# Optimization experiments

Hardware: AMD Instinct MI355X
Metric: run time of the kernel (lower is better)

Reference implementation:

```python
import jax, jax.numpy as jnp
import numpy as np

H = 1024

def _gru_layer(x_seq, W_ih, W_hh, b_ih, b_hh):
    # x_seq: [B, T, in]; W_ih: [3H, in]; W_hh: [3H, H]
    B = x_seq.shape[0]
    gx = jnp.einsum('bti,gi->btg', x_seq, W_ih) + b_ih  # [B, T, 3H] input gates precomputed

    def step(h, gx_t):
        gh = h @ W_hh.T + b_hh  # [B, 3H]
        xr, xz, xn = jnp.split(gx_t, 3, axis=-1)
        hr, hz, hn = jnp.split(gh, 3, axis=-1)
        r = jax.nn.sigmoid(xr + hr)
        z = jax.nn.sigmoid(xz + hz)
        n = jnp.tanh(xn + r * hn)
        h_new = (1.0 - z) * n + z * h
        return h_new, h_new

    h0 = jnp.zeros((B, W_hh.shape[1]), dtype=x_seq.dtype)
    _, out = jax.lax.scan(step, h0, jnp.swapaxes(gx, 0, 1))  # scan over T
    return jnp.swapaxes(out, 0, 1)  # [B, T, H]

def setup_inputs() -> dict:
    key = jax.random.key(0)
    ks = jax.random.split(key, 8)
    s = 0.03  # ~1/sqrt(H) init scale to avoid gate saturation
    return {
        'tokens': jax.random.randint(ks[0], (16, 1024), 0, 32000),
        'emb': jax.random.normal(ks[1], (32000, H), jnp.float32),
        'W_ih_l0': jax.random.normal(ks[2], (3 * H, H), jnp.float32) * s,
        'W_hh_l0': jax.random.normal(ks[3], (3 * H, H), jnp.float32) * s,
        'b_ih_l0': jnp.zeros((3 * H,), jnp.float32),
        'b_hh_l0': jnp.zeros((3 * H,), jnp.float32),
        'W_ih_l1': jax.random.normal(ks[4], (3 * H, H), jnp.float32) * s,
        'W_hh_l1': jax.random.normal(ks[5], (3 * H, H), jnp.float32) * s,
        'b_ih_l1': jnp.zeros((3 * H,), jnp.float32),
        'b_hh_l1': jnp.zeros((3 * H,), jnp.float32),
        'W_lin': jax.random.normal(ks[6], (128, H), jnp.float32) * s,
        'b_lin': jnp.zeros((128,), jnp.float32),
    }

def reference(tokens, emb, W_ih_l0, W_hh_l0, b_ih_l0, b_hh_l0,
              W_ih_l1, W_hh_l1, b_ih_l1, b_hh_l1, W_lin, b_lin):
    x = emb[tokens]  # [B, T, H]
    h1 = _gru_layer(x, W_ih_l0, W_hh_l0, b_ih_l0, b_hh_l0)
    h2 = _gru_layer(h1, W_ih_l1, W_hh_l1, b_ih_l1, b_hh_l1)
    logits = jnp.einsum('bth,ch->btc', h2, W_lin) + b_lin  # [B, T, C]
    # F.log_softmax with no dim on a 3D tensor uses dim=1 (PyTorch deprecated default)
    return jax.nn.log_softmax(logits, axis=1)
```

## Files before the change

### kernel.cpp

```cpp
#include <hip/hip_runtime.h>
#include <stdint.h>

typedef unsigned short u16;
typedef unsigned int u32;
typedef unsigned long long u64;
typedef __attribute__((ext_vector_type(8))) short short8;
typedef __attribute__((ext_vector_type(4))) float f32x4;

#define T_SEQ 1024
#define HDIM  1024
#define NG    3072
#define SLOT  16384
#define FSTRIDE 32

__device__ __forceinline__ u16 f2bf(float f) {
  unsigned u = __float_as_uint(f);
  u += 0x7FFF + ((u >> 16) & 1);
  return (u16)(u >> 16);
}
__device__ __forceinline__ float bf2f(u16 h) {
  return __uint_as_float(((unsigned)h) << 16);
}

__device__ __forceinline__ int prow(int b) { return b ^ ((b >> 2) & 1); }

__device__ __forceinline__ void gld16(void* lds, const void* g) {
  __builtin_amdgcn_global_load_lds(
      (const __attribute__((address_space(1))) unsigned*)g,
      (__attribute__((address_space(3))) unsigned*)lds, 16, 0, 0);
}

__device__ __forceinline__ void st_agent_u32(unsigned* p, unsigned v) {
  __hip_atomic_store(p, v, __ATOMIC_RELAXED, __HIP_MEMORY_SCOPE_AGENT);
}
__device__ __forceinline__ void st_agent_u64(u64* p, u64 v) {
  __hip_atomic_store(p, v, __ATOMIC_RELAXED, __HIP_MEMORY_SCOPE_AGENT);
}
__device__ __forceinline__ unsigned ld_agent_u32(const unsigned* p) {
  return __hip_atomic_load(p, __ATOMIC_RELAXED, __HIP_MEMORY_SCOPE_AGENT);
}

__device__ __forceinline__ void poll64(const unsigned* flags, int wave, int lane, unsigned need) {
  const unsigned* f = flags + (size_t)(16 * wave + (lane >> 2)) * FSTRIDE + (lane & 3);
  while (ld_agent_u32(f) < need) {}
  asm volatile("" ::: "memory");
}

__global__ void cast5_kernel(const float* __restrict__ s0, const float* __restrict__ s1,
                             const float* __restrict__ s2, const float* __restrict__ s3,
                             const float* __restrict__ s4,
                             u16* __restrict__ d0, u16* __restrict__ d1,
                             u16* __restrict__ d2, u16* __restrict__ d3,
                             u16* __restrict__ d4, unsigned* __restrict__ flags) {
  if (blockIdx.x == 0) {
#pragma unroll
    for (int k = 0; k < 64; ++k) flags[threadIdx.x * 64 + k] = 0;
  }
  int bid = blockIdx.x;
  const float* s; u16* d; size_t base;
  if (bid < 3072)       { s = s0; d = d0; base = (size_t)bid * 1024; }
  else if (bid < 6144)  { s = s1; d = d1; base = (size_t)(bid - 3072) * 1024; }
  else if (bid < 9216)  { s = s2; d = d2; base = (size_t)(bid - 6144) * 1024; }
  else if (bid < 12288) { s = s3; d = d3; base = (size_t)(bid - 9216) * 1024; }
  else                  { s = s4; d = d4; base = (size_t)(bid - 12288) * 1024; }
  size_t i = base + (size_t)threadIdx.x * 4;
  float4 v = *(const float4*)(s + i);
  unsigned lo = (unsigned)f2bf(v.x) | ((unsigned)f2bf(v.y) << 16);
  unsigned hi = (unsigned)f2bf(v.z) | ((unsigned)f2bf(v.w) << 16);
  uint2 o; o.x = lo; o.y = hi;
  *(uint2*)(d + i) = o;
}

__global__ void gather_cast_kernel(const int* __restrict__ tokens,
                                   const float* __restrict__ emb,
                                   u16* __restrict__ xbf) {
  int row = blockIdx.x;
  int tok = tokens[row];
  const float4* src = (const float4*)(emb + (size_t)tok * HDIM);
  float4 v = src[threadIdx.x];
  unsigned lo = (unsigned)f2bf(v.x) | ((unsigned)f2bf(v.y) << 16);
  unsigned hi = (unsigned)f2bf(v.z) | ((unsigned)f2bf(v.w) << 16);
  uint2 o; o.x = lo; o.y = hi;
  *(uint2*)(xbf + (size_t)row * HDIM + (size_t)threadIdx.x * 4) = o;
}

template <int OUT_MODE, bool A_PACKED, bool ADD_BIAS>
__global__ __launch_bounds__(256)
void gemm_bt(const u16* __restrict__ A, const u16* __restrict__ Bt,
             void* __restrict__ Cout, const float* __restrict__ bias,
             int M, int N) {
  const int K = 1024;
  __shared__ u16 As[128 * 32];
  __shared__ u16 Bs[128 * 32];
  const int tid = threadIdx.x;
  const int wave = tid >> 6, lane = tid & 63;
  const int quad = lane >> 4, l16 = lane & 15;
  const int wm = (wave & 1) * 64, wn = (wave >> 1) * 64;
  const int m0 = blockIdx.x * 128, n0 = blockIdx.y * 128;
  const int srow = tid >> 2, scol = (tid & 3) * 8;

  size_t abase0, abase1;
  {
    int r0 = m0 + srow, r1 = m0 + 64 + srow;
    if (A_PACKED) {
      abase0 = (size_t)((r0 & 1023) + 1) * SLOT + (size_t)(r0 >> 10) * 16 +
               (size_t)(scol & 8) + (size_t)(scol >> 4) * 256;
      abase1 = (size_t)((r1 & 1023) + 1) * SLOT + (size_t)(r1 >> 10) * 16 +
               (size_t)(scol & 8) + (size_t)(scol >> 4) * 256;
    } else {
      abase0 = (size_t)r0 * K + scol;
      abase1 = (size_t)r1 * K + scol;
    }
  }
  const size_t bbase0 = (size_t)(n0 + srow) * K + scol;
  const size_t bbase1 = (size_t)(n0 + 64 + srow) * K + scol;

  f32x4 acc[4][4] = {};

  for (int kk = 0; kk < K; kk += 32) {
    __syncthreads();
    size_t ka = A_PACKED ? (size_t)kk * 16 : (size_t)kk;
    gld16(&As[srow * 32 + scol],        A + abase0 + ka);
    gld16(&As[(64 + srow) * 32 + scol], A + abase1 + ka);
    gld16(&Bs[srow * 32 + scol],        Bt + bbase0 + kk);
    gld16(&Bs[(64 + srow) * 32 + scol], Bt + bbase1 + kk);
    __syncthreads();
    short8 af[4], bfr[4];
#pragma unroll
    for (int mt = 0; mt < 4; ++mt)
      af[mt] = *(const short8*)&As[(wm + mt * 16 + l16) * 32 + quad * 8];
#pragma unroll
    for (int nt = 0; nt < 4; ++nt)
      bfr[nt] = *(const short8*)&Bs[(wn + nt * 16 + l16) * 32 + quad * 8];
#pragma unroll
    for (int mt = 0; mt < 4; ++mt)
#pragma unroll
      for (int nt = 0; nt < 4; ++nt)
        acc[mt][nt] = __builtin_amdgcn_mfma_f32_16x16x32_bf16(af[mt], bfr[nt], acc[mt][nt], 0, 0, 0);
  }
#pragma unroll
  for (int mt = 0; mt < 4; ++mt) {
#pragma unroll
    for (int nt = 0; nt < 4; ++nt) {
#pragma unroll
      for (int r = 0; r < 4; ++r) {
        int m = m0 + wm + mt * 16 + quad * 4 + r;
        int n = n0 + wn + nt * 16 + l16;
        float v = acc[mt][nt][r];
        if (ADD_BIAS) v += bias[n];
        if (OUT_MODE == 2) {
          int t = m & 1023, b = m >> 10, g = n >> 10, c = n & 1023;
          size_t idx = ((((size_t)t * 64 + (c >> 4)) * 3 + g) * 16 + b) * 16 + (c & 15);
          ((u16*)Cout)[idx] = f2bf(v);
        } else {
          ((float*)Cout)[(size_t)m * N + n] = v;
        }
      }
    }
  }
}

__global__ __launch_bounds__(256, 1)
void fused_scan_kernel(const u16* __restrict__ gx0,
                       u16* __restrict__ h1seq, u16* __restrict__ h2seq,
                       const u16* __restrict__ Whh0, const u16* __restrict__ Wih1,
                       const u16* __restrict__ Whh1,
                       const float* __restrict__ bih0, const float* __restrict__ bhh0,
                       const float* __restrict__ bih1, const float* __restrict__ bhh1,
                       unsigned* __restrict__ flags0, unsigned* __restrict__ flags1) {
  const int tid = threadIdx.x;
  const int wave = tid >> 6, lane = tid & 63;
  const int quad = lane >> 4, l16 = lane & 15;
  const int eb = tid >> 4, ej = tid & 15;

  __shared__ float part[2][4][6][256];
  __shared__ float biasS[2][3][16];
  __shared__ u16 wx[4 * 3 * 8 * 4 * 16 * 8];

  const int fragoff = (16 * wave + (quad >> 1)) * 256 + l16 * 16 + (quad & 1) * 8;
  const int rdo = prow(eb) * 16 + ej;

  if (blockIdx.x < 64) {
    const int wg = blockIdx.x, j0 = wg * 16;
    short8 wf[3][8];
#pragma unroll
    for (int g = 0; g < 3; ++g)
#pragma unroll
      for (int s = 0; s < 8; ++s)
        wf[g][s] = *(const short8*)&Whh0[(size_t)(g * 1024 + j0 + l16) * 1024 + wave * 256 + s * 32 + quad * 8];
    if (tid < 96) {
      int a = tid / 48, rem = tid % 48, g = rem >> 4, jl = rem & 15;
      biasS[a][g][jl] = (a ? bhh0 : bih0)[g * 1024 + j0 + jl];
    }
    if (lane < 16) st_agent_u64((u64*)h1seq + wg * 64 + wave * 16 + lane, 0ull);
    asm volatile("s_waitcnt vmcnt(0)" ::: "memory");
    if (lane == 0) st_agent_u32(flags0 + (size_t)wg * FSTRIDE + wave, 1u);

    const u16* gxp = gx0 + (size_t)(wg * 3) * 256 + eb * 16 + ej;
    u16 gxu0 = gxp[0], gxu1 = gxp[256], gxu2 = gxp[512];
    float hprev = 0.f;

    for (int t = 0; t < T_SEQ; ++t) {
      const int pb = t & 1;
      poll64(flags0, wave, lane, (unsigned)(t + 1));
      const u16* src = h1seq + (size_t)t * SLOT + fragoff;
      short8 af[8];
#pragma unroll
      for (int s = 0; s < 8; ++s) af[s] = *(const short8*)(src + s * 512);
      f32x4 a0 = {0.f,0.f,0.f,0.f}, a1 = {0.f,0.f,0.f,0.f}, a2 = {0.f,0.f,0.f,0.f};
#pragma unroll
      for (int s = 0; s < 8; ++s) {
        a0 = __builtin_amdgcn_mfma_f32_16x16x32_bf16(af[s], wf[0][s], a0, 0, 0, 0);
        a1 = __builtin_amdgcn_mfma_f32_16x16x32_bf16(af[s], wf[1][s], a1, 0, 0, 0);
        a2 = __builtin_amdgcn_mfma_f32_16x16x32_bf16(af[s], wf[2][s], a2, 0, 0, 0);
      }
#pragma unroll
      for (int r = 0; r < 4; ++r) {
        int o = prow(quad * 4 + r) * 16 + l16;
        part[pb][wave][0][o] = a0[r]; part[pb][wave][1][o] = a1[r]; part[pb][wave][2][o] = a2[r];
      }
      __syncthreads();
      float ghr = part[pb][0][0][rdo] + part[pb][1][0][rdo] + part[pb][2][0][rdo] + part[pb][3][0][rdo] + biasS[1][0][ej];
      float ghz = part[pb][0][1][rdo] + part[pb][1][1][rdo] + part[pb][2][1][rdo] + part[pb][3][1][rdo] + biasS[1][1][ej];
      float ghn = part[pb][0][2][rdo] + part[pb][1][2][rdo] + part[pb][2][2][rdo] + part[pb][3][2][rdo] + biasS[1][2][ej];
      float xr = bf2f(gxu0) + biasS[0][0][ej] + ghr;
      float xz = bf2f(gxu1) + biasS[0][1][ej] + ghz;
      float xn = bf2f(gxu2) + biasS[0][2][ej];
      float r_ = 1.f / (1.f + __expf(-xr));
      float z_ = 1.f / (1.f + __expf(-xz));
      float pre = fminf(fmaxf(xn + r_ * ghn, -15.f), 15.f);
      float e2 = __expf(2.f * pre);
      float n_ = (e2 - 1.f) / (e2 + 1.f);
      float hn = (1.f - z_) * n_ + z_ * hprev;
      hprev = hn;

      unsigned mine = (unsigned)f2bf(hn);
      unsigned other = __shfl_xor(mine, 1);
      unsigned pk = mine | (other << 16);
      unsigned pk2 = __shfl_xor(pk, 2);
      if (!(tid & 3))
        st_agent_u64((u64*)h1seq + (size_t)(t + 1) * (SLOT / 4) + wg * 64 + (tid >> 2),
                     (u64)pk | ((u64)pk2 << 32));
      asm volatile("s_waitcnt vmcnt(0)" ::: "memory");
      if (lane == 0)
        st_agent_u32(flags0 + (size_t)wg * FSTRIDE + wave, (unsigned)(t + 2));
      int tn = (t + 1 < T_SEQ) ? t + 1 : t;
      const u16* gpn = gx0 + (size_t)(tn * 64 + wg) * 3 * 256 + eb * 16 + ej;
      gxu0 = gpn[0]; gxu1 = gpn[256]; gxu2 = gpn[512];
    }
  } else {
    const int wg = blockIdx.x - 64, j0 = wg * 16;
    short8 wfH[3][8];
#pragma unroll
    for (int g = 0; g < 3; ++g)
#pragma unroll
      for (int s = 0; s < 8; ++s) {
        size_t row = (size_t)(g * 1024 + j0 + l16) * 1024 + wave * 256 + s * 32 + quad * 8;
        wfH[g][s] = *(const short8*)&Whh1[row];
        short8 wv = *(const short8*)&Wih1[row];
        *(short8*)&wx[((((wave * 3 + g) * 8 + s) * 4 + quad) * 16 + l16) * 8] = wv;
      }
    if (tid < 96) {
      int a = tid / 48, rem = tid % 48, g = rem >> 4, jl = rem & 15;
      biasS[a][g][jl] = (a ? bhh1 : bih1)[g * 1024 + j0 + jl];
    }
    if (lane < 16) st_agent_u64((u64*)h2seq + wg * 64 + wave * 16 + lane, 0ull);
    asm volatile("s_waitcnt vmcnt(0)" ::: "memory");
    if (lane == 0) st_agent_u32(flags1 + (size_t)wg * FSTRIDE + wave, 1u);

    float hprev = 0.f;
    short8 af1[8];
    poll64(flags0, wave, lane, 2u);
    {
      const u16* s1 = h1seq + (size_t)SLOT + fragoff;
#pragma unroll
      for (int s = 0; s < 8; ++s) af1[s] = *(const short8*)(s1 + s * 512);
    }

    for (int t = 0; t < T_SEQ; ++t) {
      const int pb = t & 1;
      f32x4 x0 = {0.f,0.f,0.f,0.f}, x1 = {0.f,0.f,0.f,0.f}, x2 = {0.f,0.f,0.f,0.f};
#pragma unroll
      for (int s = 0; s < 8; ++s) {
        short8 w0 = *(const short8*)&wx[((((wave * 3 + 0) * 8 + s) * 4 + quad) * 16 + l16) * 8];
        short8 w1 = *(const short8*)&wx[((((wave * 3 + 1) * 8 + s) * 4 + quad) * 16 + l16) * 8];
        short8 w2 = *(const short8*)&wx[((((wave * 3 + 2) * 8 + s) * 4 + quad) * 16 + l16) * 8];
        x0 = __builtin_amdgcn_mfma_f32_16x16x32_bf16(af1[s], w0, x0, 0, 0, 0);
        x1 = __builtin_amdgcn_mfma_f32_16x16x32_bf16(af1[s], w1, x1, 0, 0, 0);
        x2 = __builtin_amdgcn_mfma_f32_16x16x32_bf16(af1[s], w2, x2, 0, 0, 0);
      }
      poll64(flags1, wave, lane, (unsigned)(t + 1));
      short8 af2[8];
      const u16* s2 = h2seq + (size_t)t * SLOT + fragoff;
#pragma unroll
      for (int s = 0; s < 8; ++s) af2[s] = *(const short8*)(s2 + s * 512);
      if (t + 1 < T_SEQ) {
        poll64(flags0, wave, lane, (unsigned)(t + 3));
        const u16* s1 = h1seq + (size_t)(t + 2) * SLOT + fragoff;
#pragma unroll
        for (int s = 0; s < 8; ++s) af1[s] = *(const short8*)(s1 + s * 512);
      }
      f32x4 h0 = {0.f,0.f,0.f,0.f}, h1a = {0.f,0.f,0.f,0.f}, h2a = {0.f,0.f,0.f,0.f};
#pragma unroll
      for (int s = 0; s < 8; ++s) {
        h0  = __builtin_amdgcn_mfma_f32_16x16x32_bf16(af2[s], wfH[0][s], h0, 0, 0, 0);
        h1a = __builtin_amdgcn_mfma_f32_16x16x32_bf16(af2[s], wfH[1][s], h1a, 0, 0, 0);
        h2a = __builtin_amdgcn_mfma_f32_16x16x32_bf16(af2[s], wfH[2][s], h2a, 0, 0, 0);
      }
#pragma unroll
      for (int r = 0; r < 4; ++r) {
        int o = prow(quad * 4 + r) * 16 + l16;
        part[pb][wave][0][o] = x0[r];  part[pb][wave][1][o] = x1[r];  part[pb][wave][2][o] = x2[r];
        part[pb][wave][3][o] = h0[r];  part[pb][wave][4][o] = h1a[r]; part[pb][wave][5][o] = h2a[r];
      }
      __syncthreads();
      float sxr = part[pb][0][0][rdo] + part[pb][1][0][rdo] + part[pb][2][0][rdo] + part[pb][3][0][rdo] + biasS[0][0][ej];
      float sxz = part[pb][0][1][rdo] + part[pb][1][1][rdo] + part[pb][2][1][rdo] + part[pb][3][1][rdo] + biasS[0][1][ej];
      float sxn = part[pb][0][2][rdo] + part[pb][1][2][rdo] + part[pb][2][2][rdo] + part[pb][3][2][rdo] + biasS[0][2][ej];
      float shr = part[pb][0][3][rdo] + part[pb][1][3][rdo] + part[pb][2][3][rdo] + part[pb][3][3][rdo] + biasS[1][0][ej];
      float shz = part[pb][0][4][rdo] + part[pb][1][4][rdo] + part[pb][2][4][rdo] + part[pb][3][4][rdo] + biasS[1][1][ej];
      float shn = part[pb][0][5][rdo] + part[pb][1][5][rdo] + part[pb][2][5][rdo] + part[pb][3][5][rdo] + biasS[1][2][ej];
      float r_ = 1.f / (1.f + __expf(-(sxr + shr)));
      float z_ = 1.f / (1.f + __expf(-(sxz + shz)));
      float pre = fminf(fmaxf(sxn + r_ * shn, -15.f), 15.f);
      float e2 = __expf(2.f * pre);
      float n_ = (e2 - 1.f) / (e2 + 1.f);
      float hn = (1.f - z_) * n_ + z_ * hprev;
      hprev = hn;

      unsigned mine = (unsigned)f2bf(hn);
      unsigned other = __shfl_xor(mine, 1);
      unsigned pk = mine | (other << 16);
      unsigned pk2 = __shfl_xor(pk, 2);
      if (!(tid & 3))
        st_agent_u64((u64*)h2seq + (size_t)(t + 1) * (SLOT / 4) + wg * 64 + (tid >> 2),
                     (u64)pk | ((u64)pk2 << 32));
      asm volatile("s_waitcnt vmcnt(0)" ::: "memory");
      if (lane == 0)
        st_agent_u32(flags1 + (size_t)wg * FSTRIDE + wave, (unsigned)(t + 2));
    }
  }
}

__global__ void logsoftmax_kernel(float* __restrict__ out) {
  int b = blockIdx.x, cg = blockIdx.y;
  int ci = threadIdx.x & 15, ts = threadIdx.x >> 4;
  int c = cg * 16 + ci;
  float m = -1e30f, s = 0.f;
  for (int t = ts; t < T_SEQ; t += 16) {
    float v = out[((size_t)b * T_SEQ + t) * 128 + c];
    if (v > m) { s = s * __expf(m - v) + 1.f; m = v; }
    else s += __expf(v - m);
  }
  __shared__ float mS[16][16], sS[16][16];
  mS[ts][ci] = m; sS[ts][ci] = s;
  __syncthreads();
  if (ts == 0) {
    float M = mS[0][ci], S = sS[0][ci];
#pragma unroll
    for (int k = 1; k < 16; ++k) {
      float m2 = mS[k][ci], s2 = sS[k][ci];
      float nm = fmaxf(M, m2);
      S = S * __expf(M - nm) + s2 * __expf(m2 - nm);
      M = nm;
    }
    sS[0][ci] = M + logf(S);
  }
  __syncthreads();
  float lsd = sS[0][ci];
  for (int t = ts; t < T_SEQ; t += 16) {
    size_t i = ((size_t)b * T_SEQ + t) * 128 + c;
    out[i] -= lsd;
  }
}

extern "C" void kernel_launch(void* const* d_in, const int* in_sizes, int n_in,
                              void* d_out, int out_size, void* d_ws, size_t ws_size,
                              hipStream_t stream) {
  const int*   tokens = (const int*)d_in[0];
  const float* emb  = (const float*)d_in[1];
  const float* Wih0 = (const float*)d_in[2];
  const float* Whh0 = (const float*)d_in[3];
  const float* bih0 = (const float*)d_in[4];
  const float* bhh0 = (const float*)d_in[5];
  const float* Wih1 = (const float*)d_in[6];
  const float* Whh1 = (const float*)d_in[7];
  const float* bih1 = (const float*)d_in[8];
  const float* bhh1 = (const float*)d_in[9];
  const float* Wlin = (const float*)d_in[10];
  const float* blin = (const float*)d_in[11];
  float* out = (float*)d_out;

  uint8_t* ws = (uint8_t*)d_ws;
  size_t off = 0;
  auto alloc = [&](size_t bytes) -> void* {
    void* p = ws + off;
    off += (bytes + 255) & ~(size_t)255;
    return p;
  };
  u16* h1seq = (u16*)alloc((size_t)(T_SEQ + 1) * SLOT * 2);
  u16* h2seq = (u16*)alloc((size_t)(T_SEQ + 1) * SLOT * 2);
  u16* gxbuf = (u16*)alloc((size_t)16384 * NG * 2);
  u16* wih0b = (u16*)alloc((size_t)NG * HDIM * 2);
  u16* whh0b = (u16*)alloc((size_t)NG * HDIM * 2);
  u16* wih1b = (u16*)alloc((size_t)NG * HDIM * 2);
  u16* whh1b = (u16*)alloc((size_t)NG * HDIM * 2);
  u16* wlinb = (u16*)alloc((size_t)128 * HDIM * 2);
  unsigned* flags = (unsigned*)alloc(65536);

  cast5_kernel<<<dim3(12416), dim3(256), 0, stream>>>(
      Wih0, Whh0, Wih1, Whh1, Wlin, wih0b, whh0b, wih1b, whh1b, wlinb, flags);
  gather_cast_kernel<<<dim3(16384), dim3(256), 0, stream>>>(tokens, emb, h1seq);
  gemm_bt<2, false, false><<<dim3(128, 24), dim3(256), 0, stream>>>(
      h1seq, wih0b, gxbuf, nullptr, 16384, NG);
  fused_scan_kernel<<<dim3(128), dim3(256), 0, stream>>>(
      gxbuf, h1seq, h2seq, whh0b, wih1b, whh1b, bih0, bhh0, bih1, bhh1,
      flags, flags + 64 * FSTRIDE);
  gemm_bt<0, true, true><<<dim3(128, 1), dim3(256), 0, stream>>>(
      h2seq, wlinb, out, blin, 16384, 128);
  logsoftmax_kernel<<<dim3(16, 8), dim3(256), 0, stream>>>(out);
}
```

Baseline: 3.134 ms.

## Publish GRU hidden state from a single wave with one flag per block

The gate epilogue now runs only in wave 0. Each lane handles 4 consecutive hidden units, reading f32x4 partial sums from LDS, and writes one packed 64-bit store. The 4-waves-per-block flags become a single flag per block, so pollers check 16 flags per wave instead of 64 and publishers issue fewer stores and flag writes. The layer-1 h2 poll and load are moved ahead of the input-projection MFMAs. The cost is serialising the epilogue onto one wave while the other three sit idle.

```diff
diff --git a/kernel.cpp b/kernel.cpp
--- a/kernel.cpp
+++ b/kernel.cpp
@@ -40,9 +40,11 @@
   return __hip_atomic_load(p, __ATOMIC_RELAXED, __HIP_MEMORY_SCOPE_AGENT);
 }
 
-__device__ __forceinline__ void poll64(const unsigned* flags, int wave, int lane, unsigned need) {
-  const unsigned* f = flags + (size_t)(16 * wave + (lane >> 2)) * FSTRIDE + (lane & 3);
-  while (ld_agent_u32(f) < need) {}
+__device__ __forceinline__ void pollW(const unsigned* flags, int wave, int lane, unsigned need) {
+  if (lane < 16) {
+    const unsigned* f = flags + (size_t)(16 * wave + lane) * FSTRIDE;
+    while (ld_agent_u32(f) < need) {}
+  }
   asm volatile("" ::: "memory");
 }
 
@@ -171,14 +173,14 @@
   const int tid = threadIdx.x;
   const int wave = tid >> 6, lane = tid & 63;
   const int quad = lane >> 4, l16 = lane & 15;
-  const int eb = tid >> 4, ej = tid & 15;
 
   __shared__ float part[2][4][6][256];
   __shared__ float biasS[2][3][16];
   __shared__ u16 wx[4 * 3 * 8 * 4 * 16 * 8];
 
   const int fragoff = (16 * wave + (quad >> 1)) * 256 + l16 * 16 + (quad & 1) * 8;
-  const int rdo = prow(eb) * 16 + ej;
+  const int pub_b = lane >> 2, pub_e4 = (lane & 3) * 4;
+  const int po = prow(pub_b) * 16 + pub_e4;
 
   if (blockIdx.x < 64) {
     const int wg = blockIdx.x, j0 = wg * 16;
@@ -192,17 +194,21 @@
       int a = tid / 48, rem = tid % 48, g = rem >> 4, jl = rem & 15;
       biasS[a][g][jl] = (a ? bhh0 : bih0)[g * 1024 + j0 + jl];
     }
-    if (lane < 16) st_agent_u64((u64*)h1seq + wg * 64 + wave * 16 + lane, 0ull);
-    asm volatile("s_waitcnt vmcnt(0)" ::: "memory");
-    if (lane == 0) st_agent_u32(flags0 + (size_t)wg * FSTRIDE + wave, 1u);
-
-    const u16* gxp = gx0 + (size_t)(wg * 3) * 256 + eb * 16 + ej;
-    u16 gxu0 = gxp[0], gxu1 = gxp[256], gxu2 = gxp[512];
-    float hprev = 0.f;
+    if (wave == 0) {
+      st_agent_u64((u64*)h1seq + wg * 64 + lane, 0ull);
+      asm volatile("s_waitcnt vmcnt(0)" ::: "memory");
+      if (lane == 0) st_agent_u32(flags0 + (size_t)wg * FSTRIDE, 1u);
+    }
+    float hp[4] = {0.f, 0.f, 0.f, 0.f};
 
     for (int t = 0; t < T_SEQ; ++t) {
       const int pb = t & 1;
-      poll64(flags0, wave, lane, (unsigned)(t + 1));
+      u64 g0 = 0, g1 = 0, g2 = 0;
+      if (wave == 0) {
+        const u64* gp = (const u64*)gx0 + ((size_t)(t * 64 + wg) * 3) * 64 + lane;
+        g0 = gp[0]; g1 = gp[64]; g2 = gp[128];
+      }
+      pollW(flags0, wave, lane, (unsigned)(t + 1));
       const u16* src = h1seq + (size_t)t * SLOT + fragoff;
       short8 af[8];
 #pragma unroll
@@ -220,33 +226,45 @@
         part[pb][wave][0][o] = a0[r]; part[pb][wave][1][o] = a1[r]; part[pb][wave][2][o] = a2[r];
       }
       __syncthreads();
-      float ghr = part[pb][0][0][rdo] + part[pb][1][0][rdo] + part[pb][2][0][rdo] + part[pb][3][0][rdo] + biasS[1][0][ej];
-      float ghz = part[pb][0][1][rdo] + part[pb][1][1][rdo] + part[pb][2][1][rdo] + part[pb][3][1][rdo] + biasS[1][1][ej];
-      float ghn = part[pb][0][2][rdo] + part[pb][1][2][rdo] + part[pb][2][2][rdo] + part[pb][3][2][rdo] + biasS[1][2][ej];
-      float xr = bf2f(gxu0) + biasS[0][0][ej] + ghr;
-      float xz = bf2f(gxu1) + biasS[0][1][ej] + ghz;
-      float xn = bf2f(gxu2) + biasS[0][2][ej];
-      float r_ = 1.f / (1.f + __expf(-xr));
-      float z_ = 1.f / (1.f + __expf(-xz));
-      float pre = fminf(fmaxf(xn + r_ * ghn, -15.f), 15.f);
-      float e2 = __expf(2.f * pre);
-      float n_ = (e2 - 1.f) / (e2 + 1.f);
-      float hn = (1.f - z_) * n_ + z_ * hprev;
-      hprev = hn;
-
-      unsigned mine = (unsigned)f2bf(hn);
-      unsigned other = __shfl_xor(mine, 1);
-      unsigned pk = mine | (other << 16);
-      unsigned pk2 = __shfl_xor(pk, 2);
-      if (!(tid & 3))
-        st_agent_u64((u64*)h1seq + (size_t)(t + 1) * (SLOT / 4) + wg * 64 + (tid >> 2),
-                     (u64)pk | ((u64)pk2 << 32));
-      asm volatile("s_waitcnt vmcnt(0)" ::: "memory");
-      if (lane == 0)
-        st_agent_u32(flags0 + (size_t)wg * FSTRIDE + wave, (unsigned)(t + 2));
-      int tn = (t + 1 < T_SEQ) ? t + 1 : t;
-      const u16* gpn = gx0 + (size_t)(tn * 64 + wg) * 3 * 256 + eb * 16 + ej;
-      gxu0 = gpn[0]; gxu1 = gpn[256]; gxu2 = gpn[512];
+      if (wave == 0) {
+        f32x4 s0 = *(const f32x4*)&part[pb][0][0][po];
+        f32x4 s1 = *(const f32x4*)&part[pb][0][1][po];
+        f32x4 s2 = *(const f32x4*)&part[pb][0][2][po];
+#pragma unroll
+        for (int w = 1; w < 4; ++w) {
+          s0 += *(const f32x4*)&part[pb][w][0][po];
+          s1 += *(const f32x4*)&part[pb][w][1][po];
+          s2 += *(const f32x4*)&part[pb][w][2][po];
+        }
+        f32x4 bh0 = *(const f32x4*)&biasS[1][0][pub_e4];
+        f32x4 bh1 = *(const f32x4*)&biasS[1][1][pub_e4];
+        f32x4 bh2 = *(const f32x4*)&biasS[1][2][pub_e4];
+        f32x4 bi0 = *(const f32x4*)&biasS[0][0][pub_e4];
+        f32x4 bi1 = *(const f32x4*)&biasS[0][1][pub_e4];
+        f32x4 bi2 = *(const f32x4*)&biasS[0][2][pub_e4];
+        u64 h64 = 0;
+#pragma unroll
+        for (int k = 0; k < 4; ++k) {
+          float ghr = s0[k] + bh0[k];
+          float ghz = s1[k] + bh1[k];
+          float ghn = s2[k] + bh2[k];
+          float xr = bf2f((u16)(g0 >> (k * 16))) + bi0[k] + ghr;
+          float xz = bf2f((u16)(g1 >> (k * 16))) + bi1[k] + ghz;
+          float xn = bf2f((u16)(g2 >> (k * 16))) + bi2[k];
+          float r_ = 1.f / (1.f + __expf(-xr));
+          float z_ = 1.f / (1.f + __expf(-xz));
+          float pre = fminf(fmaxf(xn + r_ * ghn, -15.f), 15.f);
+          float e2 = __expf(2.f * pre);
+          float n_ = (e2 - 1.f) / (e2 + 1.f);
+          float hn = (1.f - z_) * n_ + z_ * hp[k];
+          hp[k] = hn;
+          h64 |= (u64)f2bf(hn) << (k * 16);
+        }
+        st_agent_u64((u64*)h1seq + (size_t)(t + 1) * (SLOT / 4) + wg * 64 + lane, h64);
+        asm volatile("s_waitcnt vmcnt(0)" ::: "memory");
+        if (lane == 0)
+          st_agent_u32(flags0 + (size_t)wg * FSTRIDE, (unsigned)(t + 2));
+      }
     }
   } else {
     const int wg = blockIdx.x - 64, j0 = wg * 16;
@@ -264,21 +282,27 @@
       int a = tid / 48, rem = tid % 48, g = rem >> 4, jl = rem & 15;
       biasS[a][g][jl] = (a ? bhh1 : bih1)[g * 1024 + j0 + jl];
     }
-    if (lane < 16) st_agent_u64((u64*)h2seq + wg * 64 + wave * 16 + lane, 0ull);
-    asm volatile("s_waitcnt vmcnt(0)" ::: "memory");
-    if (lane == 0) st_agent_u32(flags1 + (size_t)wg * FSTRIDE + wave, 1u);
-
-    float hprev = 0.f;
+    if (wave == 0) {
+      st_agent_u64((u64*)h2seq + wg * 64 + lane, 0ull);
+      asm volatile("s_waitcnt vmcnt(0)" ::: "memory");
+      if (lane == 0) st_agent_u32(flags1 + (size_t)wg * FSTRIDE, 1u);
+    }
+    float hp[4] = {0.f, 0.f, 0.f, 0.f};
     short8 af1[8];
-    poll64(flags0, wave, lane, 2u);
+    pollW(flags0, wave, lane, 2u);
     {
-      const u16* s1 = h1seq + (size_t)SLOT + fragoff;
-#pragma unroll
-      for (int s = 0; s < 8; ++s) af1[s] = *(const short8*)(s1 + s * 512);
+      const u16* s1p = h1seq + (size_t)SLOT + fragoff;
+#pragma unroll
+      for (int s = 0; s < 8; ++s) af1[s] = *(const short8*)(s1p + s * 512);
     }
 
     for (int t = 0; t < T_SEQ; ++t) {
       const int pb = t & 1;
+      pollW(flags1, wave, lane, (unsigned)(t + 1));
+      short8 af2[8];
+      const u16* s2p = h2seq + (size_t)t * SLOT + fragoff;
+#pragma unroll
+      for (int s = 0; s < 8; ++s) af2[s] = *(const short8*)(s2p + s * 512);
       f32x4 x0 = {0.f,0.f,0.f,0.f}, x1 = {0.f,0.f,0.f,0.f}, x2 = {0.f,0.f,0.f,0.f};
 #pragma unroll
       for (int s = 0; s < 8; ++s) {
@@ -289,16 +313,11 @@
         x1 = __builtin_amdgcn_mfma_f32_16x16x32_bf16(af1[s], w1, x1, 0, 0, 0);
         x2 = __builtin_amdgcn_mfma_f32_16x16x32_bf16(af1[s], w2, x2, 0, 0, 0);
       }
-      poll64(flags1, wave, lane, (unsigned)(t + 1));
-      short8 af2[8];
-      const u16* s2 = h2seq + (size_t)t * SLOT + fragoff;
-#pragma unroll
-      for (int s = 0; s < 8; ++s) af2[s] = *(const short8*)(s2 + s * 512);
       if (t + 1 < T_SEQ) {
-        poll64(flags0, wave, lane, (unsigned)(t + 3));
-        const u16* s1 = h1seq + (size_t)(t + 2) * SLOT + fragoff;
-#pragma unroll
-        for (int s = 0; s < 8; ++s) af1[s] = *(const short8*)(s1 + s * 512);
+        pollW(flags0, wave, lane, (unsigned)(t + 3));
+        const u16* s1p = h1seq + (size_t)(t + 2) * SLOT + fragoff;
+#pragma unroll
+        for (int s = 0; s < 8; ++s) af1[s] = *(const short8*)(s1p + s * 512);
       }
       f32x4 h0 = {0.f,0.f,0.f,0.f}, h1a = {0.f,0.f,0.f,0.f}, h2a = {0.f,0.f,0.f,0.f};
 #pragma unroll
@@ -314,30 +333,51 @@
         part[pb][wave][3][o] = h0[r];  part[pb][wave][4][o] = h1a[r]; part[pb][wave][5][o] = h2a[r];
       }
       __syncthreads();
-      float sxr = part[pb][0][0][rdo] + part[pb][1][0][rdo] + part[pb][2][0][rdo] + part[pb][3][0][rdo] + biasS[0][0][ej];
-      float sxz = part[pb][0][1][rdo] + part[pb][1][1][rdo] + part[pb][2][1][rdo] + part[pb][3][1][rdo] + biasS[0][1][ej];
-      float sxn = part[pb][0][2][rdo] + part[pb][1][2][rdo] + part[pb][2][2][rdo] + part[pb][3][2][rdo] + biasS[0][2][ej];
-      float shr = part[pb][0][3][rdo] + part[pb][1][3][rdo] + part[pb][2][3][rdo] + part[pb][3][3][rdo] + biasS[1][0][ej];
-      float shz = part[pb][0][4][rdo] + part[pb][1][4][rdo] + part[pb][2][4][rdo] + part[pb][3][4][rdo] + biasS[1][1][ej];
-      float shn = part[pb][0][5][rdo] + part[pb][1][5][rdo] + part[pb][2][5][rdo] + part[pb][3][5][rdo] + biasS[1][2][ej];
-      float r_ = 1.f / (1.f + __expf(-(sxr + shr)));
-      float z_ = 1.f / (1.f + __expf(-(sxz + shz)));
-      float pre = fminf(fmaxf(sxn + r_ * shn, -15.f), 15.f);
-      float e2 = __expf(2.f * pre);
-      float n_ = (e2 - 1.f) / (e2 + 1.f);
-      float hn = (1.f - z_) * n_ + z_ * hprev;
-      hprev = hn;
-
-      unsigned mine = (unsigned)f2bf(hn);
-      unsigned other = __shfl_xor(mine, 1);
-      unsigned pk = mine | (other << 16);
-      unsigned pk2 = __shfl_xor(pk, 2);
-      if (!(tid & 3))
-        st_agent_u64((u64*)h2seq + (size_t)(t + 1) * (SLOT / 4) + wg * 64 + (tid >> 2),
-                     (u64)pk | ((u64)pk2 << 32));
-      asm volatile("s_waitcnt vmcnt(0)" ::: "memory");
-      if (lane == 0)
-        st_agent_u32(flags1 + (size_t)wg * FSTRIDE + wave, (unsigned)(t + 2));
+      if (wave == 0) {
+        f32x4 sx0 = *(const f32x4*)&part[pb][0][0][po];
+        f32x4 sx1 = *(const f32x4*)&part[pb][0][1][po];
+        f32x4 sx2 = *(const f32x4*)&part[pb][0][2][po];
+        f32x4 sh0 = *(const f32x4*)&part[pb][0][3][po];
+        f32x4 sh1 = *(const f32x4*)&part[pb][0][4][po];
+        f32x4 sh2 = *(const f32x4*)&part[pb][0][5][po];
+#pragma unroll
+        for (int w = 1; w < 4; ++w) {
+          sx0 += *(const f32x4*)&part[pb][w][0][po];
+          sx1 += *(const f32x4*)&part[pb][w][1][po];
+          sx2 += *(const f32x4*)&part[pb][w][2][po];
+          sh0 += *(const f32x4*)&part[pb][w][3][po];
+          sh1 += *(const f32x4*)&part[pb][w][4][po];
+          sh2 += *(const f32x4*)&part[pb][w][5][po];
+        }
+        f32x4 bi0 = *(const f32x4*)&biasS[0][0][pub_e4];
+        f32x4 bi1 = *(const f32x4*)&biasS[0][1][pub_e4];
+        f32x4 bi2 = *(const f32x4*)&biasS[0][2][pub_e4];
+        f32x4 bh0 = *(const f32x4*)&biasS[1][0][pub_e4];
+        f32x4 bh1 = *(const f32x4*)&biasS[1][1][pub_e4];
+        f32x4 bh2 = *(const f32x4*)&biasS[1][2][pub_e4];
+        u64 h64 = 0;
+#pragma unroll
+        for (int k = 0; k < 4; ++k) {
+          float sxr = sx0[k] + bi0[k];
+          float sxz = sx1[k] + bi1[k];
+          float sxn = sx2[k] + bi2[k];
+          float shr = sh0[k] + bh0[k];
+          float shz = sh1[k] + bh1[k];
+          float shn = sh2[k] + bh2[k];
+          float r_ = 1.f / (1.f + __expf(-(sxr + shr)));
+          float z_ = 1.f / (1.f + __expf(-(sxz + shz)));
+          float pre = fminf(fmaxf(sxn + r_ * shn, -15.f), 15.f);
+          float e2 = __expf(2.f * pre);
+          float n_ = (e2 - 1.f) / (e2 + 1.f);
+          float hn = (1.f - z_) * n_ + z_ * hp[k];
+          hp[k] = hn;
+          h64 |= (u64)f2bf(hn) << (k * 16);
+        }
+        st_agent_u64((u64*)h2seq + (size_t)(t + 1) * (SLOT / 4) + wg * 64 + lane, h64);
+        asm volatile("s_waitcnt vmcnt(0)" ::: "memory");
+        if (lane == 0)
+          st_agent_u32(flags1 + (size_t)wg * FSTRIDE, (unsigned)(t + 2));
+      }
     }
   }
 }
```

After: 3.662 ms. 16.8% more time.

## Overlap layer-0 input-gate GEMM with the recurrent scan inside the fused kernel

Applied to the files above, without the earlier changes.

Removes the standalone input-projection GEMM launch and moves its work into 128 extra blocks of the fused scan kernel. These blocks compute the gate preactivations in time chunks of 128 steps and raise a per-chunk counter. The layer-0 scan blocks spin on that counter before using each chunk. The aim is to hide the GEMM behind the serial recurrence, at the cost of a less tuned GEMM competing for CUs and bandwidth, plus the risk of a stall if the first chunk arrives late.

```diff
diff --git a/kernel.cpp b/kernel.cpp
--- a/kernel.cpp
+++ b/kernel.cpp
@@ -161,24 +161,87 @@
 }
 
 __global__ __launch_bounds__(256, 1)
-void fused_scan_kernel(const u16* __restrict__ gx0,
+void fused_scan_kernel(u16* __restrict__ gx0,
                        u16* __restrict__ h1seq, u16* __restrict__ h2seq,
                        const u16* __restrict__ Whh0, const u16* __restrict__ Wih1,
                        const u16* __restrict__ Whh1,
                        const float* __restrict__ bih0, const float* __restrict__ bhh0,
                        const float* __restrict__ bih1, const float* __restrict__ bhh1,
-                       unsigned* __restrict__ flags0, unsigned* __restrict__ flags1) {
+                       unsigned* __restrict__ flags0, unsigned* __restrict__ flags1,
+                       const u16* __restrict__ xbf, const u16* __restrict__ Wih0,
+                       unsigned* __restrict__ chunk_cnt) {
   const int tid = threadIdx.x;
   const int wave = tid >> 6, lane = tid & 63;
   const int quad = lane >> 4, l16 = lane & 15;
   const int eb = tid >> 4, ej = tid & 15;
 
-  __shared__ float part[2][4][6][256];
+  __shared__ __align__(16) float part[2][4][6][256];
   __shared__ float biasS[2][3][16];
   __shared__ u16 wx[4 * 3 * 8 * 4 * 16 * 8];
 
   const int fragoff = (16 * wave + (quad >> 1)) * 256 + l16 * 16 + (quad & 1) * 8;
   const int rdo = prow(eb) * 16 + ej;
+
+  if (blockIdx.x >= 128) {
+    const int h = blockIdx.x - 128;
+    u16* As = (u16*)&part[0][0][0][0];
+    u16* Bs = As + 128 * 32;
+    const int wm = (wave & 1) * 64, wn = (wave >> 1) * 64;
+    const int srow = tid >> 2, scol = (tid & 3) * 8;
+    for (int c = 0; c < 8; ++c) {
+#pragma unroll 1
+      for (int q3 = 0; q3 < 3; ++q3) {
+        int q = h * 3 + q3;
+        int xb = q / 24, y = q % 24;
+        int m0 = (xb * 8 + c) * 128, n0 = y * 128;
+        size_t abase0 = (size_t)(m0 + srow) * 1024 + scol;
+        size_t abase1 = (size_t)(m0 + 64 + srow) * 1024 + scol;
+        size_t bbase0 = (size_t)(n0 + srow) * 1024 + scol;
+        size_t bbase1 = (size_t)(n0 + 64 + srow) * 1024 + scol;
+        f32x4 acc[4][4] = {};
+        for (int kk = 0; kk < 1024; kk += 32) {
+          __syncthreads();
+          gld16(&As[srow * 32 + scol],        xbf + abase0 + kk);
+          gld16(&As[(64 + srow) * 32 + scol], xbf + abase1 + kk);
+          gld16(&Bs[srow * 32 + scol],        Wih0 + bbase0 + kk);
+          gld16(&Bs[(64 + srow) * 32 + scol], Wih0 + bbase1 + kk);
+          __syncthreads();
+          short8 af[4], bfr[4];
+#pragma unroll
+          for (int mt = 0; mt < 4; ++mt)
+            af[mt] = *(const short8*)&As[(wm + mt * 16 + l16) * 32 + quad * 8];
+#pragma unroll
+          for (int nt = 0; nt < 4; ++nt)
+            bfr[nt] = *(const short8*)&Bs[(wn + nt * 16 + l16) * 32 + quad * 8];
+#pragma unroll
+          for (int mt = 0; mt < 4; ++mt)
+#pragma unroll
+            for (int nt = 0; nt < 4; ++nt)
+              acc[mt][nt] = __builtin_amdgcn_mfma_f32_16x16x32_bf16(af[mt], bfr[nt], acc[mt][nt], 0, 0, 0);
+        }
+#pragma unroll
+        for (int mt = 0; mt < 4; ++mt)
+#pragma unroll
+          for (int nt = 0; nt < 4; ++nt)
+#pragma unroll
+            for (int r = 0; r < 4; ++r) {
+              int m = m0 + wm + mt * 16 + quad * 4 + r;
+              int n = n0 + wn + nt * 16 + l16;
+              unsigned v = (unsigned)f2bf(acc[mt][nt][r]);
+              unsigned other = __shfl_xor(v, 1);
+              if (!(lane & 1)) {
+                int t = m & 1023, b = m >> 10, g = n >> 10, cc = n & 1023;
+                size_t idx = ((((size_t)t * 64 + (cc >> 4)) * 3 + g) * 16 + b) * 16 + (cc & 15);
+                st_agent_u32((u32*)gx0 + (idx >> 1), v | (other << 16));
+              }
+            }
+      }
+      __syncthreads();
+      if (tid == 0)
+        __hip_atomic_fetch_add(chunk_cnt + c, 1u, __ATOMIC_RELAXED, __HIP_MEMORY_SCOPE_AGENT);
+    }
+    return;
+  }
 
   if (blockIdx.x < 64) {
     const int wg = blockIdx.x, j0 = wg * 16;
@@ -196,8 +259,13 @@
     asm volatile("s_waitcnt vmcnt(0)" ::: "memory");
     if (lane == 0) st_agent_u32(flags0 + (size_t)wg * FSTRIDE + wave, 1u);
 
-    const u16* gxp = gx0 + (size_t)(wg * 3) * 256 + eb * 16 + ej;
-    u16 gxu0 = gxp[0], gxu1 = gxp[256], gxu2 = gxp[512];
+    u16 gxu0 = 0, gxu1 = 0, gxu2 = 0;
+    {
+      if (tid == 0) { while (ld_agent_u32(chunk_cnt + 0) < 128u) {} }
+      __syncthreads();
+      const u16* gxp = gx0 + (size_t)(wg * 3) * 256 + eb * 16 + ej;
+      gxu0 = gxp[0]; gxu1 = gxp[256]; gxu2 = gxp[512];
+    }
     float hprev = 0.f;
 
     for (int t = 0; t < T_SEQ; ++t) {
@@ -245,6 +313,10 @@
       if (lane == 0)
         st_agent_u32(flags0 + (size_t)wg * FSTRIDE + wave, (unsigned)(t + 2));
       int tn = (t + 1 < T_SEQ) ? t + 1 : t;
+      if ((tn & 127) == 0 && tn != t) {
+        if (tid == 0) { while (ld_agent_u32(chunk_cnt + (tn >> 7)) < 128u) {} }
+        __syncthreads();
+      }
       const u16* gpn = gx0 + (size_t)(tn * 64 + wg) * 3 * 256 + eb * 16 + ej;
       gxu0 = gpn[0]; gxu1 = gpn[256]; gxu2 = gpn[512];
     }
@@ -400,6 +472,7 @@
   };
   u16* h1seq = (u16*)alloc((size_t)(T_SEQ + 1) * SLOT * 2);
   u16* h2seq = (u16*)alloc((size_t)(T_SEQ + 1) * SLOT * 2);
+  u16* xbf   = (u16*)alloc((size_t)16384 * HDIM * 2);
   u16* gxbuf = (u16*)alloc((size_t)16384 * NG * 2);
   u16* wih0b = (u16*)alloc((size_t)NG * HDIM * 2);
   u16* whh0b = (u16*)alloc((size_t)NG * HDIM * 2);
@@ -407,15 +480,15 @@
   u16* whh1b = (u16*)alloc((size_t)NG * HDIM * 2);
   u16* wlinb = (u16*)alloc((size_t)128 * HDIM * 2);
   unsigned* flags = (unsigned*)alloc(65536);
+  unsigned* flags1 = flags + 64 * FSTRIDE;
+  unsigned* chunk_cnt = flags + 128 * FSTRIDE;
 
   cast5_kernel<<<dim3(12416), dim3(256), 0, stream>>>(
       Wih0, Whh0, Wih1, Whh1, Wlin, wih0b, whh0b, wih1b, whh1b, wlinb, flags);
-  gather_cast_kernel<<<dim3(16384), dim3(256), 0, stream>>>(tokens, emb, h1seq);
-  gemm_bt<2, false, false><<<dim3(128, 24), dim3(256), 0, stream>>>(
-      h1seq, wih0b, gxbuf, nullptr, 16384, NG);
-  fused_scan_kernel<<<dim3(128), dim3(256), 0, stream>>>(
+  gather_cast_kernel<<<dim3(16384), dim3(256), 0, stream>>>(tokens, emb, xbf);
+  fused_scan_kernel<<<dim3(256), dim3(256), 0, stream>>>(
       gxbuf, h1seq, h2seq, whh0b, wih1b, whh1b, bih0, bhh0, bih1, bhh1,
-      flags, flags + 64 * FSTRIDE);
+      flags, flags1, xbf, wih0b, chunk_cnt);
   gemm_bt<0, true, true><<<dim3(128, 1), dim3(256), 0, stream>>>(
       h2seq, wlinb, out, blin, 16384, 128);
   logsoftmax_kernel<<<dim3(16, 8), dim3(256), 0, stream>>>(out);
```

Result: no change. 3.149 ms (+0.5%).
